# Kernel tuning notes

Hardware: AMD Instinct MI355X
Metric: run time of the kernel (lower is better)

Reference implementation:

```python
import jax, jax.numpy as jnp
import numpy as np

B, N, C_IN, HID, K, DEG = 8192, 64, 128, 128, 5, 8


def setup_inputs() -> dict:
    key = jax.random.key(0)
    ks = jax.random.split(key, 8)
    total = B * N
    E = B * N * DEG
    x = jax.random.normal(ks[0], (total, C_IN), dtype=jnp.float32)
    batch = jnp.repeat(jnp.arange(B, dtype=jnp.int64), N)
    g = jnp.repeat(jnp.arange(B, dtype=jnp.int64), N * DEG)
    src = g * N + jax.random.randint(ks[1], (E,), 0, N).astype(jnp.int64)
    dst = g * N + jax.random.randint(ks[2], (E,), 0, N).astype(jnp.int64)
    edge_index = jnp.stack([src, dst])  # [2, E]
    s = 0.05
    return {
        "x": x,
        "edge_index": edge_index,
        "batch": batch,
        "W_pool": jax.random.normal(ks[3], (C_IN, K), dtype=jnp.float32) * s,
        "b_pool": jnp.zeros((K,), jnp.float32),
        "W1": jax.random.normal(ks[4], (C_IN, HID), dtype=jnp.float32) * s,
        "b1": jnp.zeros((HID,), jnp.float32),
        "W2": jax.random.normal(ks[5], (HID, HID), dtype=jnp.float32) * s,
        "b2": jnp.zeros((HID,), jnp.float32),
        "W_lin": jax.random.normal(ks[6], (HID, 1), dtype=jnp.float32) * s,
        "b_lin": jnp.zeros((1,), jnp.float32),
        "num_graphs": B,
        "max_nodes": N,
    }


def dense_gcn(x, adj, W, b, mask=None):
    # PyG DenseGCNConv with add_loop=True: diagonal set to 1 on a copy
    n = adj.shape[1]
    idx = jnp.arange(n)
    adj_l = adj.at[:, idx, idx].set(1.0)
    out = x @ W  # [B, n, out]
    d = jnp.clip(adj_l.sum(-1), 1.0) ** -0.5  # [B, n]
    adj_n = d[:, :, None] * adj_l * d[:, None, :]
    out = jnp.einsum('bnm,bmc->bnc', adj_n, out) + b
    if mask is not None:
        out = out * mask[..., None]
    return out


def reference(x, edge_index, batch, W_pool, b_pool, W1, b1, W2, b2, W_lin, b_lin,
              num_graphs, max_nodes):
    total = x.shape[0]
    # to_dense_batch: position of each node within its graph (batch is sorted)
    first_idx = jax.ops.segment_min(jnp.arange(total), batch, num_segments=num_graphs)
    pos = jnp.arange(total) - first_idx[batch]
    x_dense = jnp.zeros((num_graphs, max_nodes, x.shape[1]), x.dtype).at[batch, pos].set(x)
    mask = jnp.zeros((num_graphs, max_nodes), x.dtype).at[batch, pos].set(1.0)
    # to_dense_adj
    src, dst = edge_index[0], edge_index[1]
    adj = jnp.zeros((num_graphs, max_nodes, max_nodes), x.dtype)
    adj = adj.at[batch[src], pos[src], pos[dst]].add(1.0)

    s = dense_gcn(x_dense, adj, W_pool, b_pool, mask)       # [B, N, K]
    x_l1 = dense_gcn(x_dense, adj, W1, b1, mask)            # [B, N, H]

    # dense_diff_pool (losses are discarded by the original forward)
    s = jax.nn.softmax(s, axis=-1) * mask[..., None]
    xm = x_l1 * mask[..., None]
    x_p1 = jnp.einsum('bnk,bnc->bkc', s, xm)                # [B, K, H]
    adj_p1 = jnp.einsum('bnk,bnm,bml->bkl', s, adj, s)      # [B, K, K]

    x_l2 = dense_gcn(x_p1, adj_p1, W2, b2)                  # [B, K, H]
    pooled = x_l2.sum(axis=1)                               # global_add_pool -> [B, H]
    return pooled @ W_lin + b_lin                           # [B, 1]
```

## Files before the change

### kernel.cpp

```cpp
#include <hip/hip_runtime.h>

#define NN 64
#define CI 128
#define HD 128
#define KC 5
#define AJW 17

#define WS_WC  0
#define WS_B1Z 768
#define WS_B2W 769

extern "C" __global__ void zprep(const float* __restrict__ W1,
                                 const float* __restrict__ Wp,
                                 const float* __restrict__ W2,
                                 const float* __restrict__ Wl,
                                 const float* __restrict__ b1,
                                 const float* __restrict__ b2,
                                 float* __restrict__ ws)
{
    const int t = threadIdx.x;
    __shared__ float sz_[HD];
    float a0 = 0.f, a1 = 0.f;
    for (int c = 0; c < HD; ++c) {
        const float wl = Wl[c];
        a0 += W2[t * HD + c] * wl;
        a1 += W2[(t + 64) * HD + c] * wl;
    }
    sz_[t] = a0; sz_[t + 64] = a1;
    float p1 = b1[t] * a0 + b1[t + 64] * a1;
    float p2 = b2[t] * Wl[t] + b2[t + 64] * Wl[t + 64];
    #pragma unroll
    for (int off = 32; off; off >>= 1) {
        p1 += __shfl_down(p1, off, 64);
        p2 += __shfl_down(p2, off, 64);
    }
    if (t == 0) { ws[WS_B1Z] = p1; ws[WS_B2W] = p2; }
    __syncthreads();
    #pragma unroll
    for (int rr = 0; rr < 2; ++rr) {
        const int r = t + rr * 64;
        float acc = 0.f;
        for (int h2 = 0; h2 < HD; ++h2) acc += W1[r * HD + h2] * sz_[h2];
        #pragma unroll
        for (int k = 0; k < KC; ++k) ws[WS_WC + r * 6 + k] = Wp[r * KC + k];
        ws[WS_WC + r * 6 + 5] = acc;
    }
}

#define EDGE(sv_, dv_) { const int s_ = (sv_) & 63, d_ = (dv_) & 63; \
    atomicAdd(&adj[s_][d_ >> 2], 1u << ((d_ & 3) * 8)); }

extern "C" __global__ __launch_bounds__(256, 6)
void diffpool_main(const float* __restrict__ x,
                   const int* __restrict__ ei,
                   const float* __restrict__ bp,
                   const float* __restrict__ bl,
                   const float* __restrict__ ws,
                   float* __restrict__ out,
                   int E, int epg, int B)
{
    __shared__ __attribute__((aligned(16))) unsigned int sadjb[4][NN][AJW];
    __shared__ __attribute__((aligned(16))) float sSm[4][NN][8];

    const int t = threadIdx.x;
    const int lane = t & 63;
    const int wv = t >> 6;
    const int g = blockIdx.x * 4 + wv;
    if (g >= B) return;

    unsigned int (*adj)[AJW] = sadjb[wv];
    float (*sm)[8] = sSm[wv];

    const int n = lane;
    const int ch = lane & 15;
    const int rg = lane >> 4;

    const float bp0 = bp[0], bp1 = bp[1], bp2 = bp[2], bp3 = bp[3], bp4 = bp[4];
    const float c_b1z = ws[WS_B1Z], c_b2w = ws[WS_B2W], c_bl = bl[0];

    const int base = g * epg;
    int4 es0, es1, ed0, ed1;
    const bool fast = (epg == 512);
    if (fast) {
        es0 = *reinterpret_cast<const int4*>(ei + base + lane * 8);
        es1 = *reinterpret_cast<const int4*>(ei + base + lane * 8 + 4);
        ed0 = *reinterpret_cast<const int4*>(ei + E + base + lane * 8);
        ed1 = *reinterpret_cast<const int4*>(ei + E + base + lane * 8 + 4);
    }

    #pragma unroll
    for (int i = 0; i < AJW; ++i) adj[lane][i] = 0u;

    if (fast) {
        EDGE(es0.x, ed0.x); EDGE(es0.y, ed0.y); EDGE(es0.z, ed0.z); EDGE(es0.w, ed0.w);
        EDGE(es1.x, ed1.x); EDGE(es1.y, ed1.y); EDGE(es1.z, ed1.z); EDGE(es1.w, ed1.w);
    } else {
        for (int j = lane; j < epg; j += 64) {
            const int sn = ei[base + j] & 63;
            const int dn = ei[E + base + j] & 63;
            atomicAdd(&adj[sn][dn >> 2], 1u << ((dn & 3) * 8));
        }
    }

    {
        float wc[48];
        const float4* wc4 = reinterpret_cast<const float4*>(ws + WS_WC + ch * 48);
        #pragma unroll
        for (int i4 = 0; i4 < 12; ++i4)
            *reinterpret_cast<float4*>(&wc[i4 * 4]) = wc4[i4];
        const float* xg = x + (size_t)g * (NN * CI);
        #pragma unroll 4
        for (int i = 0; i < 16; ++i) {
            const int row = rg + 4 * i;
            const float* xr = xg + row * CI + ch * 8;
            const float4 v0 = *reinterpret_cast<const float4*>(xr);
            const float4 v1 = *reinterpret_cast<const float4*>(xr + 4);
            float acc[6];
            #pragma unroll
            for (int k = 0; k < 6; ++k)
                acc[k] = v0.x * wc[0*6+k] + v0.y * wc[1*6+k] + v0.z * wc[2*6+k] + v0.w * wc[3*6+k]
                       + v1.x * wc[4*6+k] + v1.y * wc[5*6+k] + v1.z * wc[6*6+k] + v1.w * wc[7*6+k];
            #pragma unroll
            for (int k = 0; k < 6; ++k) {
                float r = acc[k];
                r += __shfl_xor(r, 1, 16);
                r += __shfl_xor(r, 2, 16);
                r += __shfl_xor(r, 4, 16);
                r += __shfl_xor(r, 8, 16);
                acc[k] = r;
            }
            float val = acc[0];
            #pragma unroll
            for (int k = 1; k < 6; ++k) val = (ch == k) ? acc[k] : val;
            if (ch < 6)      sm[row][ch] = val;
            else if (ch < 8) sm[row][ch] = 0.f;
        }
    }

    unsigned w[16];
    #pragma unroll
    for (int i = 0; i < 16; ++i) w[i] = adj[n][i];
    unsigned acc1 = 0u, acc2 = 0u;
    #pragma unroll
    for (int i = 0; i < 16; ++i) {
        acc1 += w[i] & 0x00FF00FFu;
        acc2 += (w[i] >> 8) & 0x00FF00FFu;
    }
    const unsigned rowsum = (acc1 & 0xFFFFu) + (acc1 >> 16) + (acc2 & 0xFFFFu) + (acc2 >> 16);
    const unsigned selfb = (adj[n][n >> 2] >> ((n & 3) * 8)) & 255u;
    const float dlane = rsqrtf((float)(rowsum + 1u - selfb));
    sm[n][6] = dlane;

    float a0 = 0.f, a1 = 0.f, a2 = 0.f, a3 = 0.f, a4 = 0.f, cp = 0.f;
    #pragma unroll
    for (int i = 0; i < 16; ++i) {
        #pragma unroll
        for (int b = 0; b < 4; ++b) {
            const int m = i * 4 + b;
            float al = (float)((w[i] >> (b * 8)) & 255u);
            al = (m == n) ? 1.f : al;
            const float4 s01 = *reinterpret_cast<const float4*>(&sm[m][0]);
            const float4 s23 = *reinterpret_cast<const float4*>(&sm[m][4]);
            const float f = al * s23.z;
            a0 += f * s01.x; a1 += f * s01.y; a2 += f * s01.z; a3 += f * s01.w;
            a4 += f * s23.x;
            cp += f * s23.y;
        }
    }

    a0 = a0 * dlane + bp0; a1 = a1 * dlane + bp1; a2 = a2 * dlane + bp2;
    a3 = a3 * dlane + bp3; a4 = a4 * dlane + bp4;
    const float mx = fmaxf(fmaxf(fmaxf(a0, a1), fmaxf(a2, a3)), a4);
    a0 = expf(a0 - mx); a1 = expf(a1 - mx); a2 = expf(a2 - mx);
    a3 = expf(a3 - mx); a4 = expf(a4 - mx);
    const float inv = 1.f / (a0 + a1 + a2 + a3 + a4);
    float sv[5];
    sv[0] = a0 * inv; sv[1] = a1 * inv; sv[2] = a2 * inv; sv[3] = a3 * inv; sv[4] = a4 * inv;
    {
        float4 s01; s01.x = sv[0]; s01.y = sv[1]; s01.z = sv[2]; s01.w = sv[3];
        *reinterpret_cast<float4*>(&sm[n][0]) = s01;
        sm[n][4] = sv[4];
    }

    float uv[5] = {0.f, 0.f, 0.f, 0.f, 0.f};
    #pragma unroll
    for (int i = 0; i < 16; ++i) {
        #pragma unroll
        for (int b = 0; b < 4; ++b) {
            const int m = i * 4 + b;
            const float c = (float)((w[i] >> (b * 8)) & 255u);
            const float4 s03 = *reinterpret_cast<const float4*>(&sm[m][0]);
            const float s4r = sm[m][4];
            uv[0] += c * s03.x; uv[1] += c * s03.y; uv[2] += c * s03.z;
            uv[3] += c * s03.w; uv[4] += c * s4r;
        }
    }

    float pr[25];
    #pragma unroll
    for (int k = 0; k < 5; ++k)
        #pragma unroll
        for (int l = 0; l < 5; ++l)
            pr[k * 5 + l] = sv[k] * uv[l];
    #pragma unroll
    for (int p = 0; p < 25; ++p) {
        float r = pr[p];
        r += __shfl_xor(r, 1, 64);
        r += __shfl_xor(r, 2, 64);
        r += __shfl_xor(r, 4, 64);
        r += __shfl_xor(r, 8, 64);
        r += __shfl_xor(r, 16, 64);
        r += __shfl_xor(r, 32, 64);
        pr[p] = r;
    }

    float d2[5], cf[5];
    #pragma unroll
    for (int k = 0; k < 5; ++k) {
        float s_ = pr[k*5+0] + pr[k*5+1] + pr[k*5+2] + pr[k*5+3] + pr[k*5+4];
        s_ += 1.f - pr[k * 6];
        d2[k] = rsqrtf(fmaxf(s_, 1.f));
    }
    #pragma unroll
    for (int l = 0; l < 5; ++l) {
        float a = 0.f;
        #pragma unroll
        for (int k = 0; k < 5; ++k) a += d2[k] * pr[k * 5 + l];
        a += d2[l] * (1.f - pr[l * 6]);
        cf[l] = d2[l] * a;
    }
    const float t5 = cf[0]*sv[0] + cf[1]*sv[1] + cf[2]*sv[2] + cf[3]*sv[3] + cf[4]*sv[4];
    float v  = (dlane * t5) * cp;
    float cb = t5;
    #pragma unroll
    for (int off = 32; off; off >>= 1) {
        v  += __shfl_down(v,  off, 64);
        cb += __shfl_down(cb, off, 64);
    }
    if (lane == 0)
        out[g] = v + cb * c_b1z + 5.f * c_b2w + c_bl;
}

extern "C" void kernel_launch(void* const* d_in, const int* in_sizes, int n_in,
                              void* d_out, int out_size, void* d_ws, size_t ws_size,
                              hipStream_t stream) {
    const float* x  = (const float*)d_in[0];
    const int*   ei = (const int*)d_in[1];
    const float* Wp = (const float*)d_in[3];
    const float* bp = (const float*)d_in[4];
    const float* W1 = (const float*)d_in[5];
    const float* b1 = (const float*)d_in[6];
    const float* W2 = (const float*)d_in[7];
    const float* b2 = (const float*)d_in[8];
    const float* Wl = (const float*)d_in[9];
    const float* bl = (const float*)d_in[10];
    float* out = (float*)d_out;
    float* ws  = (float*)d_ws;

    const int B = out_size;
    const int E = in_sizes[1] / 2;
    const int epg = E / B;

    zprep<<<1, 64, 0, stream>>>(W1, Wp, W2, Wl, b1, b2, ws);
    const int nb = (B + 3) / 4;
    diffpool_main<<<nb, 256, 0, stream>>>(x, ei, bp, bl, ws, out, E, epg, B);
}
```

Baseline: 456.1 us.

## Stage x rows into LDS via async global_load_lds in chunks

The per-wave read of the 64x128 node-feature tile now goes through direct global-to-LDS loads in four 16-row chunks instead of direct register float4 loads. The first chunk is issued before the adjacency atomics so the transfer overlaps edge scattering. Later chunks are issued only after the current one has been consumed. The launch-bounds occupancy hint drops from 6 to 2 blocks, and each wave uses an extra 8 KB of LDS, which can limit how many blocks fit per CU. The chunks are single-buffered with full vmcnt waits, so only the first chunk overlaps other work.

```diff
diff --git a/kernel.cpp b/kernel.cpp
--- a/kernel.cpp
+++ b/kernel.cpp
@@ -9,6 +9,14 @@
 #define WS_WC  0
 #define WS_B1Z 768
 #define WS_B2W 769
+
+typedef unsigned int u32;
+typedef __attribute__((address_space(1))) const u32* gas_p;
+typedef __attribute__((address_space(3))) u32* las_p;
+
+__device__ __forceinline__ void gload_lds16(const void* g, void* l) {
+    __builtin_amdgcn_global_load_lds((gas_p)g, (las_p)l, 16, 0, 0);
+}
 
 extern "C" __global__ void zprep(const float* __restrict__ W1,
                                  const float* __restrict__ Wp,
@@ -50,7 +58,7 @@
 #define EDGE(sv_, dv_) { const int s_ = (sv_) & 63, d_ = (dv_) & 63; \
     atomicAdd(&adj[s_][d_ >> 2], 1u << ((d_ & 3) * 8)); }
 
-extern "C" __global__ __launch_bounds__(256, 6)
+extern "C" __global__ __launch_bounds__(256, 2)
 void diffpool_main(const float* __restrict__ x,
                    const int* __restrict__ ei,
                    const float* __restrict__ bp,
@@ -59,6 +67,7 @@
                    float* __restrict__ out,
                    int E, int epg, int B)
 {
+    __shared__ __attribute__((aligned(16))) float sx[4][16][CI];
     __shared__ __attribute__((aligned(16))) unsigned int sadjb[4][NN][AJW];
     __shared__ __attribute__((aligned(16))) float sSm[4][NN][8];
 
@@ -70,6 +79,7 @@
 
     unsigned int (*adj)[AJW] = sadjb[wv];
     float (*sm)[8] = sSm[wv];
+    float* sxw = &sx[wv][0][0];
 
     const int n = lane;
     const int ch = lane & 15;
@@ -91,6 +101,11 @@
     #pragma unroll
     for (int i = 0; i < AJW; ++i) adj[lane][i] = 0u;
 
+    const char* xgb = (const char*)(x + (size_t)g * (NN * CI));
+    #pragma unroll
+    for (int k = 0; k < 8; ++k)
+        gload_lds16(xgb + k * 1024 + (lane << 4), sxw + k * 256);
+
     if (fast) {
         EDGE(es0.x, ed0.x); EDGE(es0.y, ed0.y); EDGE(es0.z, ed0.z); EDGE(es0.w, ed0.w);
         EDGE(es1.x, ed1.x); EDGE(es1.y, ed1.y); EDGE(es1.z, ed1.z); EDGE(es1.w, ed1.w);
@@ -102,19 +117,23 @@
         }
     }
 
+    float wc[48];
     {
-        float wc[48];
         const float4* wc4 = reinterpret_cast<const float4*>(ws + WS_WC + ch * 48);
         #pragma unroll
         for (int i4 = 0; i4 < 12; ++i4)
             *reinterpret_cast<float4*>(&wc[i4 * 4]) = wc4[i4];
-        const float* xg = x + (size_t)g * (NN * CI);
-        #pragma unroll 4
-        for (int i = 0; i < 16; ++i) {
-            const int row = rg + 4 * i;
-            const float* xr = xg + row * CI + ch * 8;
-            const float4 v0 = *reinterpret_cast<const float4*>(xr);
-            const float4 v1 = *reinterpret_cast<const float4*>(xr + 4);
+    }
+
+    #pragma unroll
+    for (int c = 0; c < 4; ++c) {
+        asm volatile("s_waitcnt vmcnt(0)" ::: "memory");
+        #pragma unroll
+        for (int i = 0; i < 4; ++i) {
+            const int rl = rg + 4 * i;
+            const int row = c * 16 + rl;
+            const float4 v0 = *reinterpret_cast<const float4*>(&sxw[rl * CI + ch * 8]);
+            const float4 v1 = *reinterpret_cast<const float4*>(&sxw[rl * CI + ch * 8 + 4]);
             float acc[6];
             #pragma unroll
             for (int k = 0; k < 6; ++k)
@@ -134,6 +153,12 @@
             for (int k = 1; k < 6; ++k) val = (ch == k) ? acc[k] : val;
             if (ch < 6)      sm[row][ch] = val;
             else if (ch < 8) sm[row][ch] = 0.f;
+        }
+        asm volatile("s_waitcnt lgkmcnt(0)" ::: "memory");
+        if (c < 3) {
+            #pragma unroll
+            for (int k = 0; k < 8; ++k)
+                gload_lds16(xgb + (c + 1) * 8192 + k * 1024 + (lane << 4), sxw + k * 256);
         }
     }
 
```

New measurement: 438.6 us. -3.8%, faster.
